# Performance work log

Measured on AMD Instinct MI355X. Metric: run time of the kernel, lower is better.

## Reference

```python
import jax, jax.numpy as jnp
import numpy as np

B, SQ, SK, D = 8, 2048, 768, 768  # SK must equal D for layer_combine concat to typecheck


def setup_inputs() -> dict:
    key = jax.random.key(0)
    ks = jax.random.split(key, 13)
    s = 0.02
    return {
        "query": jax.random.normal(ks[0], (B, SQ, D), jnp.float32),
        "key_matrix": jax.random.normal(ks[1], (B, SK, D), jnp.float32),
        "value_matrix": jax.random.normal(ks[2], (B, SK, D), jnp.float32),
        "prev_layer": jax.random.normal(ks[3], (SK, D), jnp.float32) * s,
        "attention_mask": jax.random.randint(ks[4], (B, 1, SK), 0, 2, jnp.int32),
        "Wq": jax.random.normal(ks[5], (D, D), jnp.float32) * s,
        "bq": jax.random.normal(ks[6], (D,), jnp.float32) * s,
        "Wk": jax.random.normal(ks[7], (D, D), jnp.float32) * s,
        "bk": jax.random.normal(ks[8], (D,), jnp.float32) * s,
        "Wv": jax.random.normal(ks[9], (D, D), jnp.float32) * s,
        "bv": jax.random.normal(ks[10], (D,), jnp.float32) * s,
        "Wc": jax.random.normal(ks[11], (D, 2 * D), jnp.float32) * s,
        "bc": jax.random.normal(ks[12], (D,), jnp.float32) * s,
    }


def reference(query, key_matrix, value_matrix, prev_layer, attention_mask,
              Wq, bq, Wk, bk, Wv, bv, Wc, bc):
    # Linear projections (torch Linear: x @ W.T + b)
    Q = query @ Wq.T + bq                      # [B, SQ, D]
    K = key_matrix @ Wk.T + bk                 # [B, SK, D]
    V = value_matrix @ Wv.T + bv               # computed but unused when prev_layer given (faithful)
    scale = 1.0 / np.sqrt(D).astype(np.float32)
    scores = jnp.einsum('bqd,bkd->bqk', Q, K) * scale  # [B, SQ, SK]
    scores = jnp.where(attention_mask == 0, jnp.float32(-1e9), scores)
    # prev-layer integration: matmul + concat + linear combine
    layer_attn = scores @ prev_layer           # [B, SQ, D]
    combined = jnp.concatenate([scores, layer_attn], axis=-1)  # [B, SQ, 2D]
    out = combined @ Wc.T + bc                 # [B, SQ, D]
    return out
```

## Files before the change

### kernel.cpp

```cpp
#include <hip/hip_runtime.h>
#include <hip/hip_bf16.h>


typedef __attribute__((ext_vector_type(8))) short short8;
typedef __attribute__((ext_vector_type(4))) float f32x4;
typedef __attribute__((ext_vector_type(4))) unsigned int u32x4;

#define SCALE 0.03608439182435161f

__device__ inline unsigned short f2bf(float x) {
  unsigned int u = __builtin_bit_cast(unsigned int, x);
  u = (u + 0x7fffu + ((u >> 16) & 1u)) >> 16;
  return (unsigned short)u;
}
__device__ inline float bf2f(unsigned short h) {
  return __builtin_bit_cast(float, ((unsigned int)h) << 16);
}
__device__ inline unsigned int pack_trunc(float hi, float lo) {
  return __builtin_amdgcn_perm(__builtin_bit_cast(unsigned int, hi),
                               __builtin_bit_cast(unsigned int, lo), 0x07060302u);
}

__global__ void k_prep(const float* __restrict__ prev, const float* __restrict__ Wc,
                       unsigned short* __restrict__ prev_bf,
                       unsigned short* __restrict__ Wc2_bf) {
  int g = blockIdx.x;
  int region = g / 576;
  int idx = (g - region * 576) * 256 + threadIdx.x;
  float4 v;
  unsigned short* dst;
  if (region == 0) { v = reinterpret_cast<const float4*>(prev)[idx]; dst = prev_bf; }
  else {
    int r = idx / 192, c4 = (idx - r * 192) * 4;
    v = *reinterpret_cast<const float4*>(Wc + (long long)r * 1536 + 768 + c4);
    dst = Wc2_bf;
  }
  reinterpret_cast<ushort4*>(dst)[idx] = make_ushort4(f2bf(v.x), f2bf(v.y), f2bf(v.z), f2bf(v.w));
}

__global__ void k_tposeW(const float* __restrict__ Wq, const float* __restrict__ Wk,
                         unsigned short* __restrict__ WqT, unsigned short* __restrict__ WkT) {
  __shared__ float t[64][65];
  const float* src = blockIdx.z ? Wk : Wq;
  unsigned short* dst = blockIdx.z ? WkT : WqT;
  int bx = blockIdx.x * 64, by = blockIdx.y * 64;
  int tx = threadIdx.x & 63, ty = threadIdx.x >> 6;
  #pragma unroll
  for (int i = 0; i < 64; i += 4)
    t[ty + i][tx] = src[(long long)(by + ty + i) * 768 + bx + tx];
  __syncthreads();
  #pragma unroll
  for (int i = 0; i < 64; i += 4)
    dst[(long long)(bx + ty + i) * 768 + by + tx] = f2bf(t[tx][ty + i]);
}

__global__ void k_cvtz(const float* __restrict__ key, const int* __restrict__ mask,
                       unsigned short* __restrict__ keyzT) {
  __shared__ float t[64][65];
  int b = blockIdx.z;
  const float* src = key + (long long)b * 589824;
  unsigned short* dst = keyzT + (long long)b * 589824;
  const int* mb = mask + b * 768;
  int bx = blockIdx.x * 64, by = blockIdx.y * 64;
  int tx = threadIdx.x & 63, ty = threadIdx.x >> 6;
  #pragma unroll
  for (int i = 0; i < 64; i += 4) {
    float v = src[(long long)(by + ty + i) * 768 + bx + tx];
    t[ty + i][tx] = mb[by + ty + i] ? v : 0.0f;
  }
  __syncthreads();
  #pragma unroll
  for (int i = 0; i < 64; i += 4)
    dst[(long long)(bx + ty + i) * 768 + by + tx] = f2bf(t[tx][ty + i]);
}

__global__ void k_scalars(const unsigned short* __restrict__ WqT,
                          const unsigned short* __restrict__ WkT,
                          const float* __restrict__ bk, const float* __restrict__ bq,
                          float* __restrict__ u, float* __restrict__ w3) {
  int gw = blockIdx.x * 4 + (threadIdx.x >> 6);
  int lane = threadIdx.x & 63;
  if (gw >= 1536) return;
  const unsigned short* wrow = (gw < 768) ? (WqT + (long long)gw * 768)
                                          : (WkT + (long long)(gw - 768) * 768);
  const float* vec = (gw < 768) ? bk : bq;
  float s = 0.f;
  for (int j = lane; j < 768; j += 64) s += bf2f(wrow[j]) * vec[j];
  #pragma unroll
  for (int off = 32; off > 0; off >>= 1) s += __shfl_down(s, off, 64);
  if (lane == 0) { if (gw < 768) u[gw] = s; else w3[gw - 768] = s; }
}

__global__ void k_scol(const float* __restrict__ Mt, const int* __restrict__ mask,
                       float* __restrict__ s1, float* __restrict__ sm0) {
  int gw = blockIdx.x * 4 + (threadIdx.x >> 6);
  int lane = threadIdx.x & 63;
  int b = gw / 768, d2 = gw - b * 768;
  if (b >= 8) return;
  const int* mb = mask + b * 768;
  const float* mrow = Mt + (long long)d2 * 768;
  float a1 = 0.f, a0 = 0.f;
  for (int k = lane; k < 768; k += 64) {
    float v = mrow[k];
    if (mb[k]) a1 += v; else a0 += v;
  }
  #pragma unroll
  for (int off = 32; off > 0; off >>= 1) {
    a1 += __shfl_down(a1, off, 64);
    a0 += __shfl_down(a0, off, 64);
  }
  if (lane == 0) { s1[gw] = a1; sm0[gw] = a0; }
}

__global__ void k_row(const unsigned short* __restrict__ Tt, const float* __restrict__ w3,
                      const float* __restrict__ s1, const float* __restrict__ sm0,
                      const float* __restrict__ bq, const float* __restrict__ bk,
                      const float* __restrict__ bc, float* __restrict__ row) {
  int gw = blockIdx.x * 4 + (threadIdx.x >> 6);
  int lane = threadIdx.x & 63;
  int b = gw / 768, d2 = gw - b * 768;
  if (b >= 8) return;
  const unsigned short* trow = Tt + ((long long)b * 768 + d2) * 768;
  float st = 0.f, sbb = 0.f;
  for (int j = lane; j < 768; j += 64) {
    st += bf2f(trow[j]) * w3[j];
    sbb += bq[j] * bk[j];
  }
  #pragma unroll
  for (int off = 32; off > 0; off >>= 1) {
    st += __shfl_down(st, off, 64);
    sbb += __shfl_down(sbb, off, 64);
  }
  if (lane == 0)
    row[gw] = bc[d2] - 1e9f * sm0[gw] + SCALE * (st + sbb * s1[gw]);
}

template <int MODE, int BM, int BN, int AF32>
__global__ __launch_bounds__(256) void gemm_nt(
    const void* __restrict__ A, long long aStr, int lda,
    const unsigned short* __restrict__ B, long long bStr, int ldb,
    float* __restrict__ Cf, unsigned short* __restrict__ Cbf,
    long long cStr, int ldc,
    const float* __restrict__ aux, const float* __restrict__ aux2)
{
  constexpr int BK = 64;
  constexpr int MI = BM / 32, NJ = BN / 32;
  constexpr int AGT = AF32 ? (BM * 16 / 256) : (BM * 8 / 256);
  constexpr int BGT = BN * 8 / 256;
  __shared__ __align__(16) char As[BM * BK * (AF32 ? 4 : 2)];
  __shared__ __align__(16) char Bs[BN * BK * 2];

  const int gx = gridDim.x, gy = gridDim.y;
  const int nwg = gx * gy * (int)gridDim.z;
  int lin = blockIdx.x + gx * (blockIdx.y + gy * blockIdx.z);
  int qq = nwg >> 3, rr = nwg & 7, xcd = lin & 7, loc = lin >> 3;
  int swz = (xcd < rr ? xcd * (qq + 1) : rr * (qq + 1) + (xcd - rr) * qq) + loc;
  int bz = swz / (gx * gy);
  int rem = swz - bz * gx * gy;
  int by = rem / gx, bx = rem - by * gx;

  const int b = bz;
  const int m0 = by * BM, n0 = bx * BN;
  const unsigned short* Ab16 = (const unsigned short*)A + (long long)b * aStr;
  const float*          Abf  = (const float*)A + (long long)b * aStr;
  const unsigned short* Bb = B + (long long)b * bStr;

  const int tid = threadIdx.x;
  const int w = tid >> 6, lane = tid & 63;
  const int wr = w >> 1, wc = w & 1;
  const int fr = lane & 15, fq = lane >> 4;

  f32x4 acc[MI][NJ] = {};

  for (int kt = 0; kt < 768; kt += BK) {
    __syncthreads();
    if constexpr (AF32) {
      #pragma unroll
      for (int t = 0; t < AGT; ++t) {
        int D = t * 256 + tid;
        int pr = D >> 3, slot = D & 7;
        int r = pr >> 1, h = pr & 1;
        int sg = (slot - r) & 7;
        const float* ga = Abf + (long long)(m0 + r) * lda + kt + h * 32 + sg * 4;
        __builtin_amdgcn_global_load_lds(
            (const __attribute__((address_space(1))) void*)ga,
            (__attribute__((address_space(3))) void*)(As + D * 16), 16, 0, 0);
      }
    } else {
      #pragma unroll
      for (int t = 0; t < AGT; ++t) {
        int g = t * 256 + tid;
        int row = g >> 3, s = g & 7;
        int sg = (s - row) & 7;
        const unsigned short* ga = Ab16 + (long long)(m0 + row) * lda + kt + sg * 8;
        __builtin_amdgcn_global_load_lds(
            (const __attribute__((address_space(1))) void*)ga,
            (__attribute__((address_space(3))) void*)(As + g * 16), 16, 0, 0);
      }
    }
    #pragma unroll
    for (int t = 0; t < BGT; ++t) {
      int g = t * 256 + tid;
      int row = g >> 3, s = g & 7;
      int sg = (s - row) & 7;
      const unsigned short* gb = Bb + (long long)(n0 + row) * ldb + kt + sg * 8;
      __builtin_amdgcn_global_load_lds(
          (const __attribute__((address_space(1))) void*)gb,
          (__attribute__((address_space(3))) void*)(Bs + g * 16), 16, 0, 0);
    }
    __syncthreads();

    #pragma unroll
    for (int kk = 0; kk < 2; ++kk) {
      short8 af[MI], bfr[NJ];
      #pragma unroll
      for (int i = 0; i < MI; ++i) {
        int r = wr * (BM / 2) + i * 16 + fr;
        if constexpr (AF32) {
          int pr = 2 * r + kk;
          int s0 = (fq * 2 + r) & 7;
          int s1g = (fq * 2 + 1 + r) & 7;
          f32x4 x = *reinterpret_cast<const f32x4*>(As + pr * 128 + s0 * 16);
          f32x4 y = *reinterpret_cast<const f32x4*>(As + pr * 128 + s1g * 16);
          u32x4 u4 = {pack_trunc(x[1], x[0]), pack_trunc(x[3], x[2]),
                      pack_trunc(y[1], y[0]), pack_trunc(y[3], y[2])};
          af[i] = __builtin_bit_cast(short8, u4);
        } else {
          int sgi = ((kk * 4 + fq) + r) & 7;
          af[i] = *reinterpret_cast<const short8*>(As + r * 128 + sgi * 16);
        }
      }
      #pragma unroll
      for (int j = 0; j < NJ; ++j) {
        int r = wc * (BN / 2) + j * 16 + fr;
        int sgj = ((kk * 4 + fq) + r) & 7;
        bfr[j] = *reinterpret_cast<const short8*>(Bs + r * 128 + sgj * 16);
      }
      #pragma unroll
      for (int i = 0; i < MI; ++i)
        #pragma unroll
        for (int j = 0; j < NJ; ++j)
          acc[i][j] = __builtin_amdgcn_mfma_f32_16x16x32_bf16(af[i], bfr[j], acc[i][j], 0, 0, 0);
    }
  }

  #pragma unroll
  for (int i = 0; i < MI; ++i)
    #pragma unroll
    for (int j = 0; j < NJ; ++j)
      #pragma unroll
      for (int r = 0; r < 4; ++r) {
        int row = m0 + wr * (BM / 2) + i * 16 + fq * 4 + r;
        int col = n0 + wc * (BN / 2) + j * 16 + fr;
        float v = acc[i][j][r];
        if constexpr (MODE == 0) {
          v += aux[(long long)row * 1536 + col];
          Cf[(long long)row * 768 + col] = v;
          Cbf[(long long)row * 768 + col] = f2bf(v);
        } else if constexpr (MODE == 2) {
          Cbf[(long long)b * cStr + (long long)row * ldc + col] = f2bf(v);
        } else if constexpr (MODE == 5) {
          v += aux[b * 768 + row] * aux2[col];
          Cbf[(long long)b * cStr + (long long)row * ldc + col] = f2bf(v);
        } else {
          Cf[(long long)b * cStr + (long long)row * ldc + col] = v * SCALE + aux[b * 768 + col];
        }
      }
}

extern "C" void kernel_launch(void* const* d_in, const int* in_sizes, int n_in,
                              void* d_out, int out_size, void* d_ws, size_t ws_size,
                              hipStream_t stream)
{
  const float* query = (const float*)d_in[0];
  const float* key   = (const float*)d_in[1];
  const float* prev  = (const float*)d_in[3];
  const int*   mask  = (const int*)d_in[4];
  const float* Wq    = (const float*)d_in[5];
  const float* bq    = (const float*)d_in[6];
  const float* Wk    = (const float*)d_in[7];
  const float* bk    = (const float*)d_in[8];
  const float* Wc    = (const float*)d_in[11];
  const float* bc    = (const float*)d_in[12];
  float* out = (float*)d_out;

  char* p = (char*)d_ws;
  size_t off = 0;
  auto alloc = [&](size_t bytes) {
    char* r = p + off;
    off += (bytes + 255) & ~(size_t)255;
    return r;
  };
  unsigned short* keyzT_bf = (unsigned short*)alloc(4718592ull * 2);
  unsigned short* WqT_bf   = (unsigned short*)alloc(589824ull * 2);
  unsigned short* WkT_bf   = (unsigned short*)alloc(589824ull * 2);
  unsigned short* prev_bf  = (unsigned short*)alloc(589824ull * 2);
  unsigned short* Wc2_bf   = (unsigned short*)alloc(589824ull * 2);
  float*          Mt_f     = (float*)alloc(589824ull * 4);
  unsigned short* Mt_bf    = (unsigned short*)alloc(589824ull * 2);
  unsigned short* W2_bf    = (unsigned short*)alloc(589824ull * 2);
  unsigned short* Tt_bf    = (unsigned short*)alloc(4718592ull * 2);
  unsigned short* Pt_bf    = (unsigned short*)alloc(4718592ull * 2);
  float*          s1f      = (float*)alloc(6144ull * 4);
  float*          sm0f     = (float*)alloc(6144ull * 4);
  float*          uv       = (float*)alloc(768ull * 4);
  float*          w3v      = (float*)alloc(768ull * 4);
  float*          rowv     = (float*)alloc(6144ull * 4);
  (void)ws_size; (void)in_sizes; (void)n_in; (void)out_size;

  k_tposeW<<<dim3(12, 12, 2), dim3(256), 0, stream>>>(Wq, Wk, WqT_bf, WkT_bf);
  k_prep<<<dim3(1152), dim3(256), 0, stream>>>(prev, Wc, prev_bf, Wc2_bf);
  k_cvtz<<<dim3(12, 12, 8), dim3(256), 0, stream>>>(key, mask, keyzT_bf);

  gemm_nt<0, 64, 64, 0><<<dim3(12, 12, 1), dim3(256), 0, stream>>>(
      (const void*)Wc2_bf, 0ll, 768, prev_bf, 0ll, 768, Mt_f, Mt_bf, 0ll, 768,
      Wc, (const float*)nullptr);
  gemm_nt<2, 64, 64, 0><<<dim3(12, 12, 1), dim3(256), 0, stream>>>(
      (const void*)WqT_bf, 0ll, 768, WkT_bf, 0ll, 768, (float*)nullptr, W2_bf, 0ll, 768,
      (const float*)nullptr, (const float*)nullptr);
  k_scalars<<<dim3(384), dim3(256), 0, stream>>>(WqT_bf, WkT_bf, bk, bq, uv, w3v);
  k_scol<<<dim3(1536), dim3(256), 0, stream>>>(Mt_f, mask, s1f, sm0f);
  gemm_nt<2, 64, 64, 0><<<dim3(12, 12, 8), dim3(256), 0, stream>>>(
      (const void*)Mt_bf, 0ll, 768, keyzT_bf, 589824ll, 768, (float*)nullptr, Tt_bf,
      589824ll, 768, (const float*)nullptr, (const float*)nullptr);
  gemm_nt<5, 64, 64, 0><<<dim3(12, 12, 8), dim3(256), 0, stream>>>(
      (const void*)Tt_bf, 589824ll, 768, W2_bf, 0ll, 768, (float*)nullptr, Pt_bf,
      589824ll, 768, s1f, uv);
  k_row<<<dim3(1536), dim3(256), 0, stream>>>(Tt_bf, w3v, s1f, sm0f, bq, bk, bc, rowv);
  gemm_nt<4, 128, 128, 1><<<dim3(6, 16, 8), dim3(256), 0, stream>>>(
      (const void*)query, 1572864ll, 768, Pt_bf, 589824ll, 768, out,
      (unsigned short*)nullptr, 1572864ll, 768, rowv, (const float*)nullptr);
}
```

Before: 124.7 us.

## Pre-convert query to bf16 and use double-buffered 256x192 pipelined final GEMM

Adds a separate pass that converts the fp32 query to bf16 in workspace, and replaces the final fp32-A GEMM (128x128 tiles, in-LDS fp32 packing) with a new 512-thread kernel. The new kernel uses 256x192 tiles, double-buffered LDS and global loads issued between MFMA phases, with setprio and barriers, so memory traffic overlaps compute. This removes the per-tile fp32-to-bf16 packing and halves LDS traffic for A. In exchange it adds a full extra read and write of query, and the 256-block grid with one block per CU may limit occupancy. The generic GEMM template is simplified to fixed 64x64 bf16 tiles.

```diff
diff --git a/kernel.cpp b/kernel.cpp
--- a/kernel.cpp
+++ b/kernel.cpp
@@ -4,7 +4,6 @@
 
 typedef __attribute__((ext_vector_type(8))) short short8;
 typedef __attribute__((ext_vector_type(4))) float f32x4;
-typedef __attribute__((ext_vector_type(4))) unsigned int u32x4;
 
 #define SCALE 0.03608439182435161f
 
@@ -16,9 +15,12 @@
 __device__ inline float bf2f(unsigned short h) {
   return __builtin_bit_cast(float, ((unsigned int)h) << 16);
 }
-__device__ inline unsigned int pack_trunc(float hi, float lo) {
-  return __builtin_amdgcn_perm(__builtin_bit_cast(unsigned int, hi),
-                               __builtin_bit_cast(unsigned int, lo), 0x07060302u);
+
+__global__ void k_cvt(const float* __restrict__ s, unsigned short* __restrict__ d, int n4) {
+  int i = blockIdx.x * 256 + threadIdx.x;
+  if (i >= n4) return;
+  float4 v = reinterpret_cast<const float4*>(s)[i];
+  reinterpret_cast<ushort4*>(d)[i] = make_ushort4(f2bf(v.x), f2bf(v.y), f2bf(v.z), f2bf(v.w));
 }
 
 __global__ void k_prep(const float* __restrict__ prev, const float* __restrict__ Wc,
@@ -135,19 +137,16 @@
     row[gw] = bc[d2] - 1e9f * sm0[gw] + SCALE * (st + sbb * s1[gw]);
 }
 
-template <int MODE, int BM, int BN, int AF32>
+template <int MODE>
 __global__ __launch_bounds__(256) void gemm_nt(
-    const void* __restrict__ A, long long aStr, int lda,
+    const unsigned short* __restrict__ A, long long aStr, int lda,
     const unsigned short* __restrict__ B, long long bStr, int ldb,
     float* __restrict__ Cf, unsigned short* __restrict__ Cbf,
     long long cStr, int ldc,
     const float* __restrict__ aux, const float* __restrict__ aux2)
 {
-  constexpr int BK = 64;
-  constexpr int MI = BM / 32, NJ = BN / 32;
-  constexpr int AGT = AF32 ? (BM * 16 / 256) : (BM * 8 / 256);
-  constexpr int BGT = BN * 8 / 256;
-  __shared__ __align__(16) char As[BM * BK * (AF32 ? 4 : 2)];
+  constexpr int BM = 64, BN = 64, BK = 64;
+  __shared__ __align__(16) char As[BM * BK * 2];
   __shared__ __align__(16) char Bs[BN * BK * 2];
 
   const int gx = gridDim.x, gy = gridDim.y;
@@ -160,46 +159,31 @@
   int by = rem / gx, bx = rem - by * gx;
 
   const int b = bz;
+  const unsigned short* Ab = A + (long long)b * aStr;
+  const unsigned short* Bb = B + (long long)b * bStr;
   const int m0 = by * BM, n0 = bx * BN;
-  const unsigned short* Ab16 = (const unsigned short*)A + (long long)b * aStr;
-  const float*          Abf  = (const float*)A + (long long)b * aStr;
-  const unsigned short* Bb = B + (long long)b * bStr;
 
   const int tid = threadIdx.x;
   const int w = tid >> 6, lane = tid & 63;
   const int wr = w >> 1, wc = w & 1;
   const int fr = lane & 15, fq = lane >> 4;
 
-  f32x4 acc[MI][NJ] = {};
+  f32x4 acc[2][2] = {};
 
   for (int kt = 0; kt < 768; kt += BK) {
     __syncthreads();
-    if constexpr (AF32) {
-      #pragma unroll
-      for (int t = 0; t < AGT; ++t) {
-        int D = t * 256 + tid;
-        int pr = D >> 3, slot = D & 7;
-        int r = pr >> 1, h = pr & 1;
-        int sg = (slot - r) & 7;
-        const float* ga = Abf + (long long)(m0 + r) * lda + kt + h * 32 + sg * 4;
-        __builtin_amdgcn_global_load_lds(
-            (const __attribute__((address_space(1))) void*)ga,
-            (__attribute__((address_space(3))) void*)(As + D * 16), 16, 0, 0);
-      }
-    } else {
-      #pragma unroll
-      for (int t = 0; t < AGT; ++t) {
-        int g = t * 256 + tid;
-        int row = g >> 3, s = g & 7;
-        int sg = (s - row) & 7;
-        const unsigned short* ga = Ab16 + (long long)(m0 + row) * lda + kt + sg * 8;
-        __builtin_amdgcn_global_load_lds(
-            (const __attribute__((address_space(1))) void*)ga,
-            (__attribute__((address_space(3))) void*)(As + g * 16), 16, 0, 0);
-      }
-    }
-    #pragma unroll
-    for (int t = 0; t < BGT; ++t) {
+    #pragma unroll
+    for (int t = 0; t < 2; ++t) {
+      int g = t * 256 + tid;
+      int row = g >> 3, s = g & 7;
+      int sg = (s - row) & 7;
+      const unsigned short* ga = Ab + (long long)(m0 + row) * lda + kt + sg * 8;
+      __builtin_amdgcn_global_load_lds(
+          (const __attribute__((address_space(1))) void*)ga,
+          (__attribute__((address_space(3))) void*)(As + g * 16), 16, 0, 0);
+    }
+    #pragma unroll
+    for (int t = 0; t < 2; ++t) {
       int g = t * 256 + tid;
       int row = g >> 3, s = g & 7;
       int sg = (s - row) & 7;
@@ -212,46 +196,35 @@
 
     #pragma unroll
     for (int kk = 0; kk < 2; ++kk) {
-      short8 af[MI], bfr[NJ];
-      #pragma unroll
-      for (int i = 0; i < MI; ++i) {
-        int r = wr * (BM / 2) + i * 16 + fr;
-        if constexpr (AF32) {
-          int pr = 2 * r + kk;
-          int s0 = (fq * 2 + r) & 7;
-          int s1g = (fq * 2 + 1 + r) & 7;
-          f32x4 x = *reinterpret_cast<const f32x4*>(As + pr * 128 + s0 * 16);
-          f32x4 y = *reinterpret_cast<const f32x4*>(As + pr * 128 + s1g * 16);
-          u32x4 u4 = {pack_trunc(x[1], x[0]), pack_trunc(x[3], x[2]),
-                      pack_trunc(y[1], y[0]), pack_trunc(y[3], y[2])};
-          af[i] = __builtin_bit_cast(short8, u4);
-        } else {
-          int sgi = ((kk * 4 + fq) + r) & 7;
-          af[i] = *reinterpret_cast<const short8*>(As + r * 128 + sgi * 16);
-        }
+      short8 af[2], bfr[2];
+      #pragma unroll
+      for (int i = 0; i < 2; ++i) {
+        int r = wr * 32 + i * 16 + fr;
+        int sgi = ((kk * 4 + fq) + r) & 7;
+        af[i] = *reinterpret_cast<const short8*>(As + r * 128 + sgi * 16);
       }
       #pragma unroll
-      for (int j = 0; j < NJ; ++j) {
-        int r = wc * (BN / 2) + j * 16 + fr;
+      for (int j = 0; j < 2; ++j) {
+        int r = wc * 32 + j * 16 + fr;
         int sgj = ((kk * 4 + fq) + r) & 7;
         bfr[j] = *reinterpret_cast<const short8*>(Bs + r * 128 + sgj * 16);
       }
       #pragma unroll
-      for (int i = 0; i < MI; ++i)
+      for (int i = 0; i < 2; ++i)
         #pragma unroll
-        for (int j = 0; j < NJ; ++j)
+        for (int j = 0; j < 2; ++j)
           acc[i][j] = __builtin_amdgcn_mfma_f32_16x16x32_bf16(af[i], bfr[j], acc[i][j], 0, 0, 0);
     }
   }
 
   #pragma unroll
-  for (int i = 0; i < MI; ++i)
-    #pragma unroll
-    for (int j = 0; j < NJ; ++j)
+  for (int i = 0; i < 2; ++i)
+    #pragma unroll
+    for (int j = 0; j < 2; ++j)
       #pragma unroll
       for (int r = 0; r < 4; ++r) {
-        int row = m0 + wr * (BM / 2) + i * 16 + fq * 4 + r;
-        int col = n0 + wc * (BN / 2) + j * 16 + fr;
+        int row = m0 + wr * 32 + i * 16 + fq * 4 + r;
+        int col = n0 + wc * 32 + j * 16 + fr;
         float v = acc[i][j][r];
         if constexpr (MODE == 0) {
           v += aux[(long long)row * 1536 + col];
@@ -259,12 +232,163 @@
           Cbf[(long long)row * 768 + col] = f2bf(v);
         } else if constexpr (MODE == 2) {
           Cbf[(long long)b * cStr + (long long)row * ldc + col] = f2bf(v);
-        } else if constexpr (MODE == 5) {
+        } else {
           v += aux[b * 768 + row] * aux2[col];
           Cbf[(long long)b * cStr + (long long)row * ldc + col] = f2bf(v);
-        } else {
-          Cf[(long long)b * cStr + (long long)row * ldc + col] = v * SCALE + aux[b * 768 + col];
         }
+      }
+}
+
+__global__ __launch_bounds__(512, 1) void g5_pipe(
+    const unsigned short* __restrict__ A,
+    const unsigned short* __restrict__ B,
+    float* __restrict__ C, const float* __restrict__ rowv)
+{
+  __shared__ __align__(16) char As[2][256 * 128];
+  __shared__ __align__(16) char Bs[2][192 * 128];
+
+  int lin = blockIdx.x + 4 * (blockIdx.y + 8 * blockIdx.z);
+  int swz = (lin & 7) * 32 + (lin >> 3);
+  int bz = swz >> 5;
+  int rem = swz & 31;
+  int by = rem >> 2, bx = rem & 3;
+
+  const int b = bz;
+  const int m0 = by * 256, n0 = bx * 192;
+  const unsigned short* Ab = A + (long long)b * 1572864;
+  const unsigned short* Bb = B + (long long)b * 589824;
+
+  const int tid = threadIdx.x;
+  const int w = tid >> 6, lane = tid & 63;
+  const int wr = w >> 2, wn = w & 3;
+  const int fr = lane & 15, fq = lane >> 4;
+
+  f32x4 acc[8][3] = {};
+
+  auto stageA = [&](int buf, int kt, int s0, int ns) {
+    for (int s = s0; s < s0 + ns; ++s) {
+      int g = s * 512 + tid;
+      int row = g >> 3, slot = g & 7;
+      int sg = (slot - row) & 7;
+      const unsigned short* ga = Ab + (long long)(m0 + row) * 768 + kt + sg * 8;
+      __builtin_amdgcn_global_load_lds(
+          (const __attribute__((address_space(1))) void*)ga,
+          (__attribute__((address_space(3))) void*)(&As[buf][0] + g * 16), 16, 0, 0);
+    }
+  };
+  auto stageB = [&](int buf, int kt, int s0, int ns) {
+    for (int s = s0; s < s0 + ns; ++s) {
+      int g = s * 512 + tid;
+      int row = g >> 3, slot = g & 7;
+      int sg = (slot - row) & 7;
+      const unsigned short* gb = Bb + (long long)(n0 + row) * 768 + kt + sg * 8;
+      __builtin_amdgcn_global_load_lds(
+          (const __attribute__((address_space(1))) void*)gb,
+          (__attribute__((address_space(3))) void*)(&Bs[buf][0] + g * 16), 16, 0, 0);
+    }
+  };
+
+  stageA(0, 0, 0, 4);
+  stageB(0, 0, 0, 3);
+  asm volatile("s_waitcnt vmcnt(0)" ::: "memory");
+  __builtin_amdgcn_s_barrier();
+  __builtin_amdgcn_sched_barrier(0);
+
+  int cur = 0;
+  for (int t = 0; t < 12; ++t) {
+    const char* as = &As[cur][0];
+    const char* bs = &Bs[cur][0];
+    const int ktn = (t + 1) * 64;
+    short8 a0[4], a1[4], bb[3];
+
+    #pragma unroll
+    for (int i = 0; i < 4; ++i) {
+      int r = wr * 128 + i * 16 + fr;
+      a0[i] = *reinterpret_cast<const short8*>(as + r * 128 + (((fq) + r) & 7) * 16);
+    }
+    #pragma unroll
+    for (int j = 0; j < 3; ++j) {
+      int r = wn * 48 + j * 16 + fr;
+      bb[j] = *reinterpret_cast<const short8*>(bs + r * 128 + (((fq) + r) & 7) * 16);
+    }
+    if (t < 11) stageA(cur ^ 1, ktn, 0, 2);
+    __builtin_amdgcn_s_barrier();
+    __builtin_amdgcn_s_setprio(1);
+    #pragma unroll
+    for (int i = 0; i < 4; ++i)
+      #pragma unroll
+      for (int j = 0; j < 3; ++j)
+        acc[i][j] = __builtin_amdgcn_mfma_f32_16x16x32_bf16(a0[i], bb[j], acc[i][j], 0, 0, 0);
+    __builtin_amdgcn_s_setprio(0);
+    __builtin_amdgcn_s_barrier();
+
+    #pragma unroll
+    for (int i = 0; i < 4; ++i) {
+      int r = wr * 128 + (4 + i) * 16 + fr;
+      a1[i] = *reinterpret_cast<const short8*>(as + r * 128 + (((fq) + r) & 7) * 16);
+    }
+    if (t < 11) { stageA(cur ^ 1, ktn, 2, 2); stageB(cur ^ 1, ktn, 0, 1); }
+    __builtin_amdgcn_s_barrier();
+    __builtin_amdgcn_s_setprio(1);
+    #pragma unroll
+    for (int i = 0; i < 4; ++i)
+      #pragma unroll
+      for (int j = 0; j < 3; ++j)
+        acc[4 + i][j] = __builtin_amdgcn_mfma_f32_16x16x32_bf16(a1[i], bb[j], acc[4 + i][j], 0, 0, 0);
+    __builtin_amdgcn_s_setprio(0);
+    __builtin_amdgcn_s_barrier();
+
+    #pragma unroll
+    for (int i = 0; i < 4; ++i) {
+      int r = wr * 128 + i * 16 + fr;
+      a0[i] = *reinterpret_cast<const short8*>(as + r * 128 + (((4 + fq) + r) & 7) * 16);
+    }
+    #pragma unroll
+    for (int j = 0; j < 3; ++j) {
+      int r = wn * 48 + j * 16 + fr;
+      bb[j] = *reinterpret_cast<const short8*>(bs + r * 128 + (((4 + fq) + r) & 7) * 16);
+    }
+    if (t < 11) stageB(cur ^ 1, ktn, 1, 2);
+    __builtin_amdgcn_s_barrier();
+    __builtin_amdgcn_s_setprio(1);
+    #pragma unroll
+    for (int i = 0; i < 4; ++i)
+      #pragma unroll
+      for (int j = 0; j < 3; ++j)
+        acc[i][j] = __builtin_amdgcn_mfma_f32_16x16x32_bf16(a0[i], bb[j], acc[i][j], 0, 0, 0);
+    __builtin_amdgcn_s_setprio(0);
+    __builtin_amdgcn_s_barrier();
+
+    #pragma unroll
+    for (int i = 0; i < 4; ++i) {
+      int r = wr * 128 + (4 + i) * 16 + fr;
+      a1[i] = *reinterpret_cast<const short8*>(as + r * 128 + (((4 + fq) + r) & 7) * 16);
+    }
+    __builtin_amdgcn_s_barrier();
+    __builtin_amdgcn_s_setprio(1);
+    #pragma unroll
+    for (int i = 0; i < 4; ++i)
+      #pragma unroll
+      for (int j = 0; j < 3; ++j)
+        acc[4 + i][j] = __builtin_amdgcn_mfma_f32_16x16x32_bf16(a1[i], bb[j], acc[4 + i][j], 0, 0, 0);
+    __builtin_amdgcn_s_setprio(0);
+
+    if (t < 11) asm volatile("s_waitcnt vmcnt(0)" ::: "memory");
+    __builtin_amdgcn_s_barrier();
+    __builtin_amdgcn_sched_barrier(0);
+    cur ^= 1;
+  }
+
+  const long long ob = (long long)b * 1572864;
+  #pragma unroll
+  for (int i = 0; i < 8; ++i)
+    #pragma unroll
+    for (int j = 0; j < 3; ++j)
+      #pragma unroll
+      for (int r = 0; r < 4; ++r) {
+        int row = m0 + wr * 128 + i * 16 + fq * 4 + r;
+        int col = n0 + wn * 48 + j * 16 + fr;
+        C[ob + (long long)row * 768 + col] = acc[i][j][r] * SCALE + rowv[b * 768 + col];
       }
 }
 
@@ -291,6 +415,7 @@
     off += (bytes + 255) & ~(size_t)255;
     return r;
   };
+  unsigned short* query_bf = (unsigned short*)alloc(12582912ull * 2);
   unsigned short* keyzT_bf = (unsigned short*)alloc(4718592ull * 2);
   unsigned short* WqT_bf   = (unsigned short*)alloc(589824ull * 2);
   unsigned short* WkT_bf   = (unsigned short*)alloc(589824ull * 2);
@@ -308,26 +433,25 @@
   float*          rowv     = (float*)alloc(6144ull * 4);
   (void)ws_size; (void)in_sizes; (void)n_in; (void)out_size;
 
+  k_cvt<<<dim3(12288), dim3(256), 0, stream>>>(query, query_bf, 3145728);
   k_tposeW<<<dim3(12, 12, 2), dim3(256), 0, stream>>>(Wq, Wk, WqT_bf, WkT_bf);
   k_prep<<<dim3(1152), dim3(256), 0, stream>>>(prev, Wc, prev_bf, Wc2_bf);
   k_cvtz<<<dim3(12, 12, 8), dim3(256), 0, stream>>>(key, mask, keyzT_bf);
 
-  gemm_nt<0, 64, 64, 0><<<dim3(12, 12, 1), dim3(256), 0, stream>>>(
-      (const void*)Wc2_bf, 0ll, 768, prev_bf, 0ll, 768, Mt_f, Mt_bf, 0ll, 768,
+  gemm_nt<0><<<dim3(12, 12, 1), dim3(256), 0, stream>>>(
+      Wc2_bf, 0ll, 768, prev_bf, 0ll, 768, Mt_f, Mt_bf, 0ll, 768,
       Wc, (const float*)nullptr);
-  gemm_nt<2, 64, 64, 0><<<dim3(12, 12, 1), dim3(256), 0, stream>>>(
-      (const void*)WqT_bf, 0ll, 768, WkT_bf, 0ll, 768, (float*)nullptr, W2_bf, 0ll, 768,
+  gemm_nt<2><<<dim3(12, 12, 1), dim3(256), 0, stream>>>(
+      WqT_bf, 0ll, 768, WkT_bf, 0ll, 768, (float*)nullptr, W2_bf, 0ll, 768,
       (const float*)nullptr, (const float*)nullptr);
   k_scalars<<<dim3(384), dim3(256), 0, stream>>>(WqT_bf, WkT_bf, bk, bq, uv, w3v);
   k_scol<<<dim3(1536), dim3(256), 0, stream>>>(Mt_f, mask, s1f, sm0f);
-  gemm_nt<2, 64, 64, 0><<<dim3(12, 12, 8), dim3(256), 0, stream>>>(
-      (const void*)Mt_bf, 0ll, 768, keyzT_bf, 589824ll, 768, (float*)nullptr, Tt_bf,
+  gemm_nt<2><<<dim3(12, 12, 8), dim3(256), 0, stream>>>(
+      Mt_bf, 0ll, 768, keyzT_bf, 589824ll, 768, (float*)nullptr, Tt_bf,
       589824ll, 768, (const float*)nullptr, (const float*)nullptr);
-  gemm_nt<5, 64, 64, 0><<<dim3(12, 12, 8), dim3(256), 0, stream>>>(
-      (const void*)Tt_bf, 589824ll, 768, W2_bf, 0ll, 768, (float*)nullptr, Pt_bf,
+  gemm_nt<5><<<dim3(12, 12, 8), dim3(256), 0, stream>>>(
+      Tt_bf, 589824ll, 768, W2_bf, 0ll, 768, (float*)nullptr, Pt_bf,
       589824ll, 768, s1f, uv);
   k_row<<<dim3(1536), dim3(256), 0, stream>>>(Tt_bf, w3v, s1f, sm0f, bq, bk, bc, rowv);
-  gemm_nt<4, 128, 128, 1><<<dim3(6, 16, 8), dim3(256), 0, stream>>>(
-      (const void*)query, 1572864ll, 768, Pt_bf, 589824ll, 768, out,
-      (unsigned short*)nullptr, 1572864ll, 768, rowv, (const float*)nullptr);
-}
+  g5_pipe<<<dim3(4, 8, 8), dim3(512), 0, stream>>>(query_bf, Pt_bf, out, rowv);
+}
```

After: 121.4 us. -2.7%, faster.
